# Kernel tuning notes

Hardware: AMD Instinct MI355X
Metric: run time of the kernel (lower is better)

## Reference

```python
import jax, jax.numpy as jnp
import numpy as np

D_MODEL = 512
HIDDEN = 2 * D_MODEL
B, L = 8, 2048
R_MIN, R_MAX = 0.8, 0.99
LN_EPS = 1e-5


def setup_inputs() -> dict:
    key = jax.random.key(0)
    ks = jax.random.split(key, 12)
    x = jax.random.normal(ks[0], (B, L, D_MODEL), jnp.float32)
    mask = jnp.ones((B, L), jnp.float32)
    # LRU eigenvalue init, exactly as the torch __init__
    u1 = jax.random.uniform(ks[1], (HIDDEN,), jnp.float32)
    u2 = jax.random.uniform(ks[2], (HIDDEN,), jnp.float32)
    nu_log = jnp.log(-0.5 * jnp.log(u1 * (R_MAX ** 2 - R_MIN ** 2) + R_MIN ** 2))
    theta_log = jnp.log(u2 * 2.0 * np.pi)
    diag_lambda = jnp.exp(jax.lax.complex(-jnp.exp(nu_log), jnp.exp(theta_log)))
    gamma_log = jnp.log(jnp.sqrt(1.0 - jnp.abs(diag_lambda) ** 2))
    params_log = jnp.stack([nu_log, theta_log, gamma_log])  # (3, HIDDEN)
    s_in = 1.0 / np.sqrt(D_MODEL)
    s_out = 1.0 / np.sqrt(HIDDEN)
    # complex Linear weights (real+imag parts; trained weights are fully complex)
    W_in_re = jax.random.uniform(ks[3], (HIDDEN, D_MODEL), jnp.float32, -s_in, s_in)
    W_in_im = jax.random.uniform(ks[4], (HIDDEN, D_MODEL), jnp.float32, -s_in, s_in)
    b_in_re = jax.random.uniform(ks[5], (HIDDEN,), jnp.float32, -s_in, s_in)
    b_in_im = jax.random.uniform(ks[6], (HIDDEN,), jnp.float32, -s_in, s_in)
    W_out_re = jax.random.uniform(ks[7], (D_MODEL, HIDDEN), jnp.float32, -s_out, s_out)
    W_out_im = jax.random.uniform(ks[8], (D_MODEL, HIDDEN), jnp.float32, -s_out, s_out)
    b_out_re = jax.random.uniform(ks[9], (D_MODEL,), jnp.float32, -s_out, s_out)
    b_out_im = jax.random.uniform(ks[10], (D_MODEL,), jnp.float32, -s_out, s_out)
    ln_w = jnp.ones((D_MODEL,), jnp.float32)
    ln_b = jnp.zeros((D_MODEL,), jnp.float32)
    return dict(x=x, mask=mask, params_log=params_log,
                W_in_re=W_in_re, W_in_im=W_in_im, b_in_re=b_in_re, b_in_im=b_in_im,
                W_out_re=W_out_re, W_out_im=W_out_im, b_out_re=b_out_re, b_out_im=b_out_im,
                ln_w=ln_w, ln_b=ln_b)


def _lru_parallel_scan(h, lamb, mask, Bn, Ln, Dn):
    # log-depth doubling trick over complex diagonal recurrence (faithful port)
    log2_L = int(np.ceil(np.log2(Ln)))
    for i in range(1, log2_L + 1):
        l = 2 ** i
        h = h.reshape(Bn * Ln // l, l, Dn)
        m = mask.reshape(Bn * Ln // l, l)
        h1, h2 = h[:, : l // 2], h[:, l // 2 :]
        if i > 1:
            lamb = jnp.concatenate([lamb, lamb * lamb[-1]], axis=0)  # powers lam^1..lam^(l/2)
        h2 = h2 + lamb * h1[:, -1:] * m[:, l // 2 - 1 : l // 2, None]
        h = jnp.concatenate([h1, h2], axis=1)
    return h.reshape(Bn, Ln, Dn)


def reference(x, mask, params_log, W_in_re, W_in_im, b_in_re, b_in_im,
              W_out_re, W_out_im, b_out_re, b_out_im, ln_w, ln_b):
    nu, theta, gamma = jnp.exp(params_log)  # each (HIDDEN,)
    lamb = jnp.exp(jax.lax.complex(-nu, theta))[None, :]  # (1, HIDDEN)
    W_in = jax.lax.complex(W_in_re, W_in_im)
    b_in = jax.lax.complex(b_in_re, b_in_im)
    W_out = jax.lax.complex(W_out_re, W_out_im)
    b_out = jax.lax.complex(b_out_re, b_out_im)
    xc = x.astype(jnp.complex64)
    h = (jnp.einsum('bld,hd->blh', xc, W_in) + b_in) * gamma  # (B, L, HIDDEN) complex64
    Bn, Ln, Dn = h.shape
    h = _lru_parallel_scan(h, lamb, mask, Bn, Ln, Dn)
    y = (jnp.einsum('blh,dh->bld', h, W_out) + b_out).real + x  # dropout = identity (eval)
    mean = jnp.mean(y, axis=-1, keepdims=True)
    var = jnp.var(y, axis=-1, keepdims=True)
    return (y - mean) / jnp.sqrt(var + LN_EPS) * ln_w + ln_b
```

## Files before the change

kernel.cpp:

```cpp
#include <hip/hip_runtime.h>
#include <hip/hip_bf16.h>
#include <cstdint>
#include <cstddef>


typedef unsigned short u16;
typedef __attribute__((ext_vector_type(8))) short bf16x8;
typedef __attribute__((ext_vector_type(4))) float f32x4;

#define B_    8
#define L_    2048
#define D_    512
#define H_    1024
#define M_    (B_ * L_)
#define SEG_  64
#define T_    (L_ / SEG_)

__device__ __forceinline__ float b2f(u16 u) {
  union { unsigned int i; float f; } v; v.i = ((unsigned int)u) << 16; return v.f;
}
__device__ __forceinline__ u16 f2b(float f) {
  union { float f; unsigned int i; } v; v.f = f;
  unsigned int x = v.i;
  return (u16)((x + 0x7fffu + ((x >> 16) & 1u)) >> 16);
}

__device__ __forceinline__ void gl2lds16(const void* g, void* l) {
  __builtin_amdgcn_global_load_lds(
      (const __attribute__((address_space(1))) void*)g,
      (__attribute__((address_space(3))) void*)l, 16, 0, 0);
}

__device__ __forceinline__ int ksw(int row, int kc) {
  return (kc ^ (row & 3) ^ ((row >> 2) & 3)) & 3;
}

__global__ __launch_bounds__(256) void conv_f32_bf16(
    const float* __restrict__ in, u16* __restrict__ out, int n4)
{
  int i = blockIdx.x * 256 + threadIdx.x;
  if (i < n4) {
    float4 v = ((const float4*)in)[i];
    ushort4 o;
    o.x = f2b(v.x); o.y = f2b(v.y); o.z = f2b(v.z); o.w = f2b(v.w);
    ((ushort4*)out)[i] = o;
  }
}

__global__ __launch_bounds__(256) void prep_weights(
    const float* __restrict__ wire, const float* __restrict__ wiim,
    const float* __restrict__ wore, const float* __restrict__ woim,
    u16* __restrict__ winb, u16* __restrict__ wcat)
{
  int i = blockIdx.x * 256 + threadIdx.x;
  winb[i]                  = f2b(wire[i]);
  winb[H_ * D_ + i]        = f2b(wiim[i]);
  int d = i >> 10, c = i & 1023;
  wcat[(size_t)d * 2048 + c]        = f2b(wore[i]);
  wcat[(size_t)d * 2048 + 1024 + c] = f2b(-woim[i]);
}

template <int MODE>
__global__ __launch_bounds__(256, 4) void gemm_bt(
    const u16* __restrict__ A, const u16* __restrict__ Bp, int K,
    void* __restrict__ outp, int ldc,
    const float* __restrict__ p0, const float* __restrict__ p1,
    const float* __restrict__ p2)
{
  __shared__ __align__(16) u16 sA[128 * 32];
  __shared__ __align__(16) u16 sB[128 * 32];

  const int tid  = threadIdx.x;
  const int lane = tid & 63;
  const int wave = tid >> 6;
  const int wm = wave >> 1, wn = wave & 1;
  const int m0 = blockIdx.x * 128;
  const int n0 = blockIdx.y * 128;

  f32x4 acc[4][4];
#pragma unroll
  for (int i = 0; i < 4; ++i)
#pragma unroll
    for (int j = 0; j < 4; ++j) { f32x4 z = {0.f, 0.f, 0.f, 0.f}; acc[i][j] = z; }

  const int q = lane >> 4;
  const int r = lane & 15;

  for (int k0 = 0; k0 < K; k0 += 32) {
#pragma unroll
    for (int it = 0; it < 2; ++it) {
      int ci  = it * 256 + tid;
      int row = ci >> 2;
      int kc  = ksw(row, ci & 3);
      gl2lds16(A  + (size_t)(m0 + row) * K + k0 + kc * 8, &sA[ci * 8]);
      gl2lds16(Bp + (size_t)(n0 + row) * K + k0 + kc * 8, &sB[ci * 8]);
    }
    __syncthreads();

    bf16x8 af[4], bfv[4];
#pragma unroll
    for (int mt = 0; mt < 4; ++mt) {
      int arow = wm * 64 + mt * 16 + r;
      int slot = (arow << 2) | ksw(arow, q);
      af[mt] = *(const bf16x8*)&sA[slot * 8];
    }
#pragma unroll
    for (int nt = 0; nt < 4; ++nt) {
      int brow = wn * 64 + nt * 16 + r;
      int slot = (brow << 2) | ksw(brow, q);
      bfv[nt] = *(const bf16x8*)&sB[slot * 8];
    }
#pragma unroll
    for (int mt = 0; mt < 4; ++mt)
#pragma unroll
      for (int nt = 0; nt < 4; ++nt)
        acc[mt][nt] = __builtin_amdgcn_mfma_f32_16x16x32_bf16(
            af[mt], bfv[nt], acc[mt][nt], 0, 0, 0);
    __syncthreads();
  }

#pragma unroll
  for (int nt = 0; nt < 4; ++nt) {
    const int ng = n0 + wn * 64 + nt * 16 + r;
    float bias, gam = 1.f;
    if (MODE == 0) {
      bias = (ng < 1024) ? p0[ng] : p1[ng - 1024];
      gam  = expf(p2[2 * H_ + (ng & (H_ - 1))]);
    } else {
      bias = p0[ng];
    }
#pragma unroll
    for (int mt = 0; mt < 4; ++mt) {
      const int mg = m0 + wm * 64 + mt * 16 + q * 4;
#pragma unroll
      for (int i = 0; i < 4; ++i) {
        float v = acc[mt][nt][i] + bias;
        if (MODE == 0)
          ((u16*)outp)[(size_t)(mg + i) * ldc + ng] = f2b(v * gam);
        else
          ((float*)outp)[(size_t)(mg + i) * ldc + ng] = v;
      }
    }
  }
}

__global__ __launch_bounds__(256) void scan_fin(
    const u16* __restrict__ h, const float* __restrict__ mask,
    const float* __restrict__ params, float2* __restrict__ segfin,
    float* __restrict__ prodm)
{
  const int s = blockIdx.x, b = blockIdx.y;
  const int c4 = threadIdx.x * 4;
  float lr[4], li[4];
#pragma unroll
  for (int j = 0; j < 4; ++j) {
    int c = c4 + j;
    float nu = expf(params[c]);
    float th = expf(params[H_ + c]);
    float mg = expf(-nu);
    lr[j] = mg * cosf(th);
    li[j] = mg * sinf(th);
  }
  const int t0 = s * T_;
  const u16* p = h + (size_t)(b * L_ + t0) * (2 * H_) + c4;
  const float* mp = mask + b * L_ + t0;
  float fac0;
  if (t0 == 0) fac0 = 0.f; else fac0 = mask[b * L_ + t0 - 1];

  ushort4 bre[2][8], bim[2][8];
#pragma unroll
  for (int j = 0; j < 8; ++j) {
    bre[0][j] = *(const ushort4*)(p + (size_t)j * 2 * H_);
    bim[0][j] = *(const ushort4*)(p + (size_t)j * 2 * H_ + H_);
  }
  float sr[4] = {0, 0, 0, 0}, si[4] = {0, 0, 0, 0};
  float pm = 1.f;
#pragma unroll
  for (int ch = 0; ch < T_ / 8; ++ch) {
    const int cur = ch & 1, nxt = cur ^ 1;
    if (ch < T_ / 8 - 1) {
      const u16* pn = p + (size_t)(ch + 1) * 8 * 2 * H_;
#pragma unroll
      for (int j = 0; j < 8; ++j) {
        bre[nxt][j] = *(const ushort4*)(pn + (size_t)j * 2 * H_);
        bim[nxt][j] = *(const ushort4*)(pn + (size_t)j * 2 * H_ + H_);
      }
    }
#pragma unroll
    for (int j = 0; j < 8; ++j) {
      int i = ch * 8 + j;
      float fac = (i == 0) ? fac0 : mp[i - 1];
      pm *= fac;
      u16 rr[4], ii[4];
      *(ushort4*)rr = bre[cur][j]; *(ushort4*)ii = bim[cur][j];
#pragma unroll
      for (int k = 0; k < 4; ++k) {
        float ar = fac * sr[k], ai = fac * si[k];
        sr[k] = b2f(rr[k]) + lr[k] * ar - li[k] * ai;
        si[k] = b2f(ii[k]) + lr[k] * ai + li[k] * ar;
      }
    }
  }
#pragma unroll
  for (int j = 0; j < 4; ++j)
    segfin[(size_t)(b * SEG_ + s) * H_ + c4 + j] = make_float2(sr[j], si[j]);
  if (threadIdx.x == 0) prodm[b * SEG_ + s] = pm;
}

__global__ __launch_bounds__(256) void scan_carry(
    const float2* __restrict__ segfin, const float* __restrict__ prodm,
    const float* __restrict__ params, float2* __restrict__ carries)
{
  int idx = blockIdx.x * 256 + threadIdx.x;
  int b = idx >> 10, c = idx & 1023;
  float nu = expf(params[c]);
  float th = expf(params[H_ + c]);
  float mg = expf(-nu);
  float ltr = mg * cosf(th), lti = mg * sinf(th);
#pragma unroll
  for (int sq = 0; sq < 5; ++sq) {
    float nr = ltr * ltr - lti * lti;
    float ni = 2.f * ltr * lti;
    ltr = nr; lti = ni;
  }
  float cr = 0.f, ci = 0.f;
  for (int s = 0; s < SEG_; ++s) {
    size_t o = (size_t)(b * SEG_ + s) * H_ + c;
    carries[o] = make_float2(cr, ci);
    float2 fin = segfin[o];
    float pmv = prodm[b * SEG_ + s];
    float nr = fin.x + pmv * (ltr * cr - lti * ci);
    float ni = fin.y + pmv * (ltr * ci + lti * cr);
    cr = nr; ci = ni;
  }
}

__global__ __launch_bounds__(256) void scan_full(
    u16* __restrict__ h, const float* __restrict__ mask,
    const float* __restrict__ params, const float2* __restrict__ carries)
{
  const int s = blockIdx.x, b = blockIdx.y;
  const int c4 = threadIdx.x * 4;
  float lr[4], li[4], sr[4], si[4];
#pragma unroll
  for (int j = 0; j < 4; ++j) {
    int c = c4 + j;
    float nu = expf(params[c]);
    float th = expf(params[H_ + c]);
    float mg = expf(-nu);
    lr[j] = mg * cosf(th);
    li[j] = mg * sinf(th);
    float2 cv = carries[(size_t)(b * SEG_ + s) * H_ + c];
    sr[j] = cv.x; si[j] = cv.y;
  }
  const int t0 = s * T_;
  u16* p = h + (size_t)(b * L_ + t0) * (2 * H_) + c4;
  const float* mp = mask + b * L_ + t0;
  float fac0;
  if (t0 == 0) fac0 = 0.f; else fac0 = mask[b * L_ + t0 - 1];

  ushort4 cre = *(const ushort4*)p;
  ushort4 cim = *(const ushort4*)(p + H_);
  for (int i = 0; i < T_; ++i) {
    ushort4 nre = cre, nim = cim;
    if (i + 1 < T_) {
      nre = *(const ushort4*)(p + 2 * H_);
      nim = *(const ushort4*)(p + 2 * H_ + H_);
    }
    float fac = (i == 0) ? fac0 : mp[i - 1];
    u16 rr[4], ii[4], orr[4], oii[4];
    *(ushort4*)rr = cre; *(ushort4*)ii = cim;
#pragma unroll
    for (int j = 0; j < 4; ++j) {
      float ar = fac * sr[j], ai = fac * si[j];
      float nr2 = b2f(rr[j]) + lr[j] * ar - li[j] * ai;
      float ni2 = b2f(ii[j]) + lr[j] * ai + li[j] * ar;
      sr[j] = nr2; si[j] = ni2;
      orr[j] = f2b(nr2); oii[j] = f2b(ni2);
    }
    *(ushort4*)p        = *(ushort4*)orr;
    *(ushort4*)(p + H_) = *(ushort4*)oii;
    p += 2 * H_;
    cre = nre; cim = nim;
  }
}

__global__ __launch_bounds__(256) void ln_kernel(
    const float* __restrict__ y, const float* __restrict__ xg,
    const float* __restrict__ lnw, const float* __restrict__ lnb,
    float* __restrict__ out)
{
  const int wave = threadIdx.x >> 6, lane = threadIdx.x & 63;
  const size_t row = (size_t)blockIdx.x * 4 + wave;
  const float* yr = y + row * 512;
  const float* xr = xg + row * 512;
  float z[8];
  { float4 t = *(const float4*)&yr[lane * 4];        z[0]=t.x; z[1]=t.y; z[2]=t.z; z[3]=t.w; }
  { float4 t = *(const float4*)&yr[256 + lane * 4];  z[4]=t.x; z[5]=t.y; z[6]=t.z; z[7]=t.w; }
  { float4 t = *(const float4*)&xr[lane * 4];        z[0]+=t.x; z[1]+=t.y; z[2]+=t.z; z[3]+=t.w; }
  { float4 t = *(const float4*)&xr[256 + lane * 4];  z[4]+=t.x; z[5]+=t.y; z[6]+=t.z; z[7]+=t.w; }
  float s = 0.f, ss = 0.f;
#pragma unroll
  for (int j = 0; j < 8; ++j) { s += z[j]; ss += z[j] * z[j]; }
#pragma unroll
  for (int o = 32; o > 0; o >>= 1) { s += __shfl_xor(s, o); ss += __shfl_xor(ss, o); }
  const float mean = s * (1.f / 512.f);
  const float var  = ss * (1.f / 512.f) - mean * mean;
  const float inv  = rsqrtf(var + 1e-5f);
  float ov[8];
#pragma unroll
  for (int j = 0; j < 8; ++j) {
    int col = (j < 4) ? (lane * 4 + j) : (256 + lane * 4 + (j - 4));
    ov[j] = (z[j] - mean) * inv * lnw[col] + lnb[col];
  }
  { float4 t; t.x=ov[0]; t.y=ov[1]; t.z=ov[2]; t.w=ov[3];
    *(float4*)&out[row * 512 + lane * 4] = t; }
  { float4 t; t.x=ov[4]; t.y=ov[5]; t.z=ov[6]; t.w=ov[7];
    *(float4*)&out[row * 512 + 256 + lane * 4] = t; }
}

extern "C" void kernel_launch(void* const* d_in, const int* in_sizes, int n_in,
                              void* d_out, int out_size, void* d_ws, size_t ws_size,
                              hipStream_t stream) {
  (void)in_sizes; (void)n_in; (void)out_size; (void)ws_size;
  const float* x      = (const float*)d_in[0];
  const float* mask   = (const float*)d_in[1];
  const float* params = (const float*)d_in[2];
  const float* Wire   = (const float*)d_in[3];
  const float* Wiim   = (const float*)d_in[4];
  const float* bire   = (const float*)d_in[5];
  const float* biim   = (const float*)d_in[6];
  const float* Wore   = (const float*)d_in[7];
  const float* Woim   = (const float*)d_in[8];
  const float* bore   = (const float*)d_in[9];
  const float* lnw    = (const float*)d_in[11];
  const float* lnb    = (const float*)d_in[12];

  char* ws = (char*)d_ws;
  u16*    xb      = (u16*)   (ws);
  float2* segfin  = (float2*)(ws);
  float2* carries = (float2*)(ws + (size_t)4194304);
  float*  prodm   = (float*) (ws + (size_t)8388608);
  float*  y       = (float*) (ws);
  u16*    h       = (u16*)   (ws + (size_t)33554432);
  u16*    winb    = (u16*)   (ws + (size_t)100663296);
  u16*    wcat    = (u16*)   (ws + (size_t)102760448);

  conv_f32_bf16<<<8192, 256, 0, stream>>>(x, xb, M_ * D_ / 4);
  prep_weights<<<2048, 256, 0, stream>>>(Wire, Wiim, Wore, Woim, winb, wcat);

  gemm_bt<0><<<dim3(128, 16), 256, 0, stream>>>(
      xb, winb, 512, (void*)h, 2048, bire, biim, params);

  scan_fin<<<dim3(SEG_, B_), 256, 0, stream>>>(h, mask, params, segfin, prodm);
  scan_carry<<<32, 256, 0, stream>>>(segfin, prodm, params, carries);
  scan_full<<<dim3(SEG_, B_), 256, 0, stream>>>(h, mask, params, carries);

  gemm_bt<1><<<dim3(128, 4), 256, 0, stream>>>(
      h, wcat, 2048, (void*)y, 512, bore, nullptr, nullptr);

  ln_kernel<<<4096, 256, 0, stream>>>(y, x, lnw, lnb, (float*)d_out);
}
```

Measured before the change: 262.5 us.

## Vectorize GEMM epilogue stores, fold gamma into weights, shorten scan segments

Swaps the MFMA operands so each lane holds four consecutive output columns, which lets the GEMM epilogue emit vectorized ushort4/float4 stores instead of scalar strided ones. Gamma is folded into the input weights and bias during weight prep, so the epilogue no longer does per-column expf and bias selection. The scan segment count doubles, halving the sequential length per thread and doubling the parallel blocks. Each scan thread now preloads its whole segment and mask into registers, and scan_carry prefetches the next segment's values. The costs are a longer carry chain, larger scratch buffers, and rounding gamma into bf16 weights before the GEMM rather than after it.

```diff
diff --git a/kernel.cpp b/kernel.cpp
--- a/kernel.cpp
+++ b/kernel.cpp
@@ -13,7 +13,7 @@
 #define D_    512
 #define H_    1024
 #define M_    (B_ * L_)
-#define SEG_  64
+#define SEG_  128
 #define T_    (L_ / SEG_)
 
 __device__ __forceinline__ float b2f(u16 u) {
@@ -50,22 +50,27 @@
 __global__ __launch_bounds__(256) void prep_weights(
     const float* __restrict__ wire, const float* __restrict__ wiim,
     const float* __restrict__ wore, const float* __restrict__ woim,
-    u16* __restrict__ winb, u16* __restrict__ wcat)
+    const float* __restrict__ bire, const float* __restrict__ biim,
+    const float* __restrict__ params,
+    u16* __restrict__ winb, u16* __restrict__ wcat, float* __restrict__ bb)
 {
   int i = blockIdx.x * 256 + threadIdx.x;
-  winb[i]                  = f2b(wire[i]);
-  winb[H_ * D_ + i]        = f2b(wiim[i]);
+  float g = expf(params[2 * H_ + (i >> 9)]);
+  winb[i]           = f2b(wire[i] * g);
+  winb[H_ * D_ + i] = f2b(wiim[i] * g);
   int d = i >> 10, c = i & 1023;
   wcat[(size_t)d * 2048 + c]        = f2b(wore[i]);
   wcat[(size_t)d * 2048 + 1024 + c] = f2b(-woim[i]);
+  if (i < 2048) {
+    float gb = expf(params[2 * H_ + (i & (H_ - 1))]);
+    bb[i] = ((i < 1024) ? bire[i] : biim[i - 1024]) * gb;
+  }
 }
 
 template <int MODE>
 __global__ __launch_bounds__(256, 4) void gemm_bt(
     const u16* __restrict__ A, const u16* __restrict__ Bp, int K,
-    void* __restrict__ outp, int ldc,
-    const float* __restrict__ p0, const float* __restrict__ p1,
-    const float* __restrict__ p2)
+    void* __restrict__ outp, int ldc, const float* __restrict__ p0)
 {
   __shared__ __align__(16) u16 sA[128 * 32];
   __shared__ __align__(16) u16 sB[128 * 32];
@@ -115,30 +120,31 @@
 #pragma unroll
       for (int nt = 0; nt < 4; ++nt)
         acc[mt][nt] = __builtin_amdgcn_mfma_f32_16x16x32_bf16(
-            af[mt], bfv[nt], acc[mt][nt], 0, 0, 0);
+            bfv[nt], af[mt], acc[mt][nt], 0, 0, 0);
     __syncthreads();
   }
 
 #pragma unroll
   for (int nt = 0; nt < 4; ++nt) {
-    const int ng = n0 + wn * 64 + nt * 16 + r;
-    float bias, gam = 1.f;
-    if (MODE == 0) {
-      bias = (ng < 1024) ? p0[ng] : p1[ng - 1024];
-      gam  = expf(p2[2 * H_ + (ng & (H_ - 1))]);
-    } else {
-      bias = p0[ng];
-    }
+    const int nb = n0 + wn * 64 + nt * 16 + q * 4;
+    const float4 b4 = *(const float4*)&p0[nb];
 #pragma unroll
     for (int mt = 0; mt < 4; ++mt) {
-      const int mg = m0 + wm * 64 + mt * 16 + q * 4;
-#pragma unroll
-      for (int i = 0; i < 4; ++i) {
-        float v = acc[mt][nt][i] + bias;
-        if (MODE == 0)
-          ((u16*)outp)[(size_t)(mg + i) * ldc + ng] = f2b(v * gam);
-        else
-          ((float*)outp)[(size_t)(mg + i) * ldc + ng] = v;
+      const int mg = m0 + wm * 64 + mt * 16 + r;
+      if (MODE == 0) {
+        ushort4 o;
+        o.x = f2b(acc[mt][nt][0] + b4.x);
+        o.y = f2b(acc[mt][nt][1] + b4.y);
+        o.z = f2b(acc[mt][nt][2] + b4.z);
+        o.w = f2b(acc[mt][nt][3] + b4.w);
+        *(ushort4*)&((u16*)outp)[(size_t)mg * ldc + nb] = o;
+      } else {
+        float4 o;
+        o.x = acc[mt][nt][0] + b4.x;
+        o.y = acc[mt][nt][1] + b4.y;
+        o.z = acc[mt][nt][2] + b4.z;
+        o.w = acc[mt][nt][3] + b4.w;
+        *(float4*)&((float*)outp)[(size_t)mg * ldc + nb] = o;
       }
     }
   }
@@ -167,38 +173,30 @@
   float fac0;
   if (t0 == 0) fac0 = 0.f; else fac0 = mask[b * L_ + t0 - 1];
 
-  ushort4 bre[2][8], bim[2][8];
-#pragma unroll
-  for (int j = 0; j < 8; ++j) {
-    bre[0][j] = *(const ushort4*)(p + (size_t)j * 2 * H_);
-    bim[0][j] = *(const ushort4*)(p + (size_t)j * 2 * H_ + H_);
-  }
+  ushort4 re[T_], im[T_];
+#pragma unroll
+  for (int j = 0; j < T_; ++j) {
+    re[j] = *(const ushort4*)(p + (size_t)j * 2 * H_);
+    im[j] = *(const ushort4*)(p + (size_t)j * 2 * H_ + H_);
+  }
+  float mf[T_];
+  mf[0] = fac0;
+#pragma unroll
+  for (int j = 1; j < T_; ++j) mf[j] = mp[j - 1];
+
   float sr[4] = {0, 0, 0, 0}, si[4] = {0, 0, 0, 0};
   float pm = 1.f;
 #pragma unroll
-  for (int ch = 0; ch < T_ / 8; ++ch) {
-    const int cur = ch & 1, nxt = cur ^ 1;
-    if (ch < T_ / 8 - 1) {
-      const u16* pn = p + (size_t)(ch + 1) * 8 * 2 * H_;
-#pragma unroll
-      for (int j = 0; j < 8; ++j) {
-        bre[nxt][j] = *(const ushort4*)(pn + (size_t)j * 2 * H_);
-        bim[nxt][j] = *(const ushort4*)(pn + (size_t)j * 2 * H_ + H_);
-      }
-    }
-#pragma unroll
-    for (int j = 0; j < 8; ++j) {
-      int i = ch * 8 + j;
-      float fac = (i == 0) ? fac0 : mp[i - 1];
-      pm *= fac;
-      u16 rr[4], ii[4];
-      *(ushort4*)rr = bre[cur][j]; *(ushort4*)ii = bim[cur][j];
-#pragma unroll
-      for (int k = 0; k < 4; ++k) {
-        float ar = fac * sr[k], ai = fac * si[k];
-        sr[k] = b2f(rr[k]) + lr[k] * ar - li[k] * ai;
-        si[k] = b2f(ii[k]) + lr[k] * ai + li[k] * ar;
-      }
+  for (int i = 0; i < T_; ++i) {
+    float fac = mf[i];
+    pm *= fac;
+    u16 rr[4], ii[4];
+    *(ushort4*)rr = re[i]; *(ushort4*)ii = im[i];
+#pragma unroll
+    for (int k = 0; k < 4; ++k) {
+      float ar = fac * sr[k], ai = fac * si[k];
+      sr[k] = b2f(rr[k]) + lr[k] * ar - li[k] * ai;
+      si[k] = b2f(ii[k]) + lr[k] * ai + li[k] * ar;
     }
   }
 #pragma unroll
@@ -218,20 +216,23 @@
   float mg = expf(-nu);
   float ltr = mg * cosf(th), lti = mg * sinf(th);
 #pragma unroll
-  for (int sq = 0; sq < 5; ++sq) {
+  for (int sq = 0; sq < 4; ++sq) {
     float nr = ltr * ltr - lti * lti;
     float ni = 2.f * ltr * lti;
     ltr = nr; lti = ni;
   }
   float cr = 0.f, ci = 0.f;
+  float2 fin = segfin[(size_t)(b * SEG_) * H_ + c];
+  float pmv = prodm[b * SEG_];
   for (int s = 0; s < SEG_; ++s) {
     size_t o = (size_t)(b * SEG_ + s) * H_ + c;
     carries[o] = make_float2(cr, ci);
-    float2 fin = segfin[o];
-    float pmv = prodm[b * SEG_ + s];
+    float2 finn; float pmn;
+    if (s + 1 < SEG_) { finn = segfin[o + H_]; pmn = prodm[b * SEG_ + s + 1]; }
     float nr = fin.x + pmv * (ltr * cr - lti * ci);
     float ni = fin.y + pmv * (ltr * ci + lti * cr);
     cr = nr; ci = ni;
+    fin = finn; pmv = pmn;
   }
 }
 
@@ -259,17 +260,22 @@
   float fac0;
   if (t0 == 0) fac0 = 0.f; else fac0 = mask[b * L_ + t0 - 1];
 
-  ushort4 cre = *(const ushort4*)p;
-  ushort4 cim = *(const ushort4*)(p + H_);
+  ushort4 re[T_], im[T_];
+#pragma unroll
+  for (int j = 0; j < T_; ++j) {
+    re[j] = *(const ushort4*)(p + (size_t)j * 2 * H_);
+    im[j] = *(const ushort4*)(p + (size_t)j * 2 * H_ + H_);
+  }
+  float mf[T_];
+  mf[0] = fac0;
+#pragma unroll
+  for (int j = 1; j < T_; ++j) mf[j] = mp[j - 1];
+
+#pragma unroll
   for (int i = 0; i < T_; ++i) {
-    ushort4 nre = cre, nim = cim;
-    if (i + 1 < T_) {
-      nre = *(const ushort4*)(p + 2 * H_);
-      nim = *(const ushort4*)(p + 2 * H_ + H_);
-    }
-    float fac = (i == 0) ? fac0 : mp[i - 1];
+    float fac = mf[i];
     u16 rr[4], ii[4], orr[4], oii[4];
-    *(ushort4*)rr = cre; *(ushort4*)ii = cim;
+    *(ushort4*)rr = re[i]; *(ushort4*)ii = im[i];
 #pragma unroll
     for (int j = 0; j < 4; ++j) {
       float ar = fac * sr[j], ai = fac * si[j];
@@ -278,10 +284,8 @@
       sr[j] = nr2; si[j] = ni2;
       orr[j] = f2b(nr2); oii[j] = f2b(ni2);
     }
-    *(ushort4*)p        = *(ushort4*)orr;
-    *(ushort4*)(p + H_) = *(ushort4*)oii;
-    p += 2 * H_;
-    cre = nre; cim = nim;
+    *(ushort4*)(p + (size_t)i * 2 * H_)      = *(ushort4*)orr;
+    *(ushort4*)(p + (size_t)i * 2 * H_ + H_) = *(ushort4*)oii;
   }
 }
 
@@ -339,25 +343,27 @@
   char* ws = (char*)d_ws;
   u16*    xb      = (u16*)   (ws);
   float2* segfin  = (float2*)(ws);
-  float2* carries = (float2*)(ws + (size_t)4194304);
-  float*  prodm   = (float*) (ws + (size_t)8388608);
+  float2* carries = (float2*)(ws + (size_t)8388608);
+  float*  prodm   = (float*) (ws + (size_t)16777216);
   float*  y       = (float*) (ws);
   u16*    h       = (u16*)   (ws + (size_t)33554432);
   u16*    winb    = (u16*)   (ws + (size_t)100663296);
   u16*    wcat    = (u16*)   (ws + (size_t)102760448);
+  float*  bb      = (float*) (ws + (size_t)104857600);
 
   conv_f32_bf16<<<8192, 256, 0, stream>>>(x, xb, M_ * D_ / 4);
-  prep_weights<<<2048, 256, 0, stream>>>(Wire, Wiim, Wore, Woim, winb, wcat);
+  prep_weights<<<2048, 256, 0, stream>>>(Wire, Wiim, Wore, Woim, bire, biim,
+                                         params, winb, wcat, bb);
 
   gemm_bt<0><<<dim3(128, 16), 256, 0, stream>>>(
-      xb, winb, 512, (void*)h, 2048, bire, biim, params);
+      xb, winb, 512, (void*)h, 2048, bb);
 
   scan_fin<<<dim3(SEG_, B_), 256, 0, stream>>>(h, mask, params, segfin, prodm);
   scan_carry<<<32, 256, 0, stream>>>(segfin, prodm, params, carries);
   scan_full<<<dim3(SEG_, B_), 256, 0, stream>>>(h, mask, params, carries);
 
   gemm_bt<1><<<dim3(128, 4), 256, 0, stream>>>(
-      h, wcat, 2048, (void*)y, 512, bore, nullptr, nullptr);
+      h, wcat, 2048, (void*)y, 512, bore);
 
   ln_kernel<<<4096, 256, 0, stream>>>(y, x, lnw, lnb, (float*)d_out);
 }
```

Result: slower. 284.5 us (+8.4%).
